# Performance work log

Hardware: AMD Instinct MI355X
Metric: run time of the kernel (lower is better)

Reference implementation:

```python
import jax, jax.numpy as jnp
import numpy as np

N = 50000      # nodes
E = 800000     # edges (before self-loops)
IN = 128       # in_channels
HID = 16       # hidden_channels
HEADS = 8
OUT = 16       # out_channels
NEG_SLOPE = 0.2
BN_EPS = 1e-5
LN_EPS = 1e-5


def setup_inputs() -> dict:
    key = jax.random.key(0)
    ks = jax.random.split(key, 16)
    s = 0.05
    inp = {
        "x": jax.random.normal(ks[0], (N, IN), jnp.float32),
        "edge_index": jax.random.randint(ks[1], (2, E), 0, N, jnp.int64),
        # conv1 (in=IN, out=HID, heads=HEADS, concat=True)
        "Wl1": jax.random.normal(ks[2], (HEADS * HID, IN), jnp.float32) * s,
        "bl1": jnp.zeros((HEADS * HID,), jnp.float32),
        "Wr1": jax.random.normal(ks[3], (HEADS * HID, IN), jnp.float32) * s,
        "br1": jnp.zeros((HEADS * HID,), jnp.float32),
        "att1": jax.random.normal(ks[4], (HEADS, HID), jnp.float32) * s,
        "bias1": jnp.zeros((HEADS * HID,), jnp.float32),
        # batchnorm (eval mode, running stats)
        "bn_w": jnp.ones((HEADS * HID,), jnp.float32),
        "bn_b": jnp.zeros((HEADS * HID,), jnp.float32),
        "bn_rm": jnp.zeros((HEADS * HID,), jnp.float32),
        "bn_rv": jnp.ones((HEADS * HID,), jnp.float32),
        # conv2 (in=HEADS*HID, out=OUT, heads=HEADS, concat=False)
        "Wl2": jax.random.normal(ks[5], (HEADS * OUT, HEADS * HID), jnp.float32) * s,
        "bl2": jnp.zeros((HEADS * OUT,), jnp.float32),
        "Wr2": jax.random.normal(ks[6], (HEADS * OUT, HEADS * HID), jnp.float32) * s,
        "br2": jnp.zeros((HEADS * OUT,), jnp.float32),
        "att2": jax.random.normal(ks[7], (HEADS, OUT), jnp.float32) * s,
        "bias2": jnp.zeros((OUT,), jnp.float32),
        # skip + layernorm
        "Wskip": jax.random.normal(ks[8], (OUT, IN), jnp.float32) * s,
        "ln_w": jnp.ones((OUT,), jnp.float32),
        "ln_b": jnp.zeros((OUT,), jnp.float32),
    }
    return inp


def _gatv2(x, src, dst, Wl, bl, Wr, br, att, bias, heads, ch, concat):
    """PyG GATv2Conv (share_weights=False), eval mode (no dropout)."""
    n = x.shape[0]
    xl = (x @ Wl.T + bl).reshape(n, heads, ch)   # source transform
    xr = (x @ Wr.T + br).reshape(n, heads, ch)   # target transform
    # edge-wise attention score
    e = jax.nn.leaky_relu(xl[src] + xr[dst], NEG_SLOPE)          # [E',H,C]
    score = jnp.einsum('ehc,hc->eh', e, att)                      # [E',H]
    # segment softmax over incoming edges per destination node
    smax = jax.ops.segment_max(score, dst, num_segments=n)
    ex = jnp.exp(score - smax[dst])
    denom = jax.ops.segment_sum(ex, dst, num_segments=n)
    alpha = ex / denom[dst]                                       # [E',H]
    out = jax.ops.segment_sum(alpha[:, :, None] * xl[src], dst, num_segments=n)
    if concat:
        out = out.reshape(n, heads * ch)
    else:
        out = out.mean(axis=1)
    return out + bias


def reference(x, edge_index, Wl1, bl1, Wr1, br1, att1, bias1,
              bn_w, bn_b, bn_rm, bn_rv,
              Wl2, bl2, Wr2, br2, att2, bias2,
              Wskip, ln_w, ln_b):
    n = x.shape[0]
    loops = jnp.arange(n, dtype=edge_index.dtype)
    src = jnp.concatenate([edge_index[0], loops])
    dst = jnp.concatenate([edge_index[1], loops])

    x_res = x @ Wskip.T                                            # [N,OUT]

    h = _gatv2(x, src, dst, Wl1, bl1, Wr1, br1, att1, bias1, HEADS, HID, True)
    # BatchNorm1d in eval mode
    h = (h - bn_rm) * jax.lax.rsqrt(bn_rv + BN_EPS) * bn_w + bn_b
    h = jax.nn.elu(h)

    h = _gatv2(h, src, dst, Wl2, bl2, Wr2, br2, att2, bias2, HEADS, OUT, False)

    y = h + x_res
    mu = y.mean(axis=-1, keepdims=True)
    var = ((y - mu) ** 2).mean(axis=-1, keepdims=True)
    return (y - mu) * jax.lax.rsqrt(var + LN_EPS) * ln_w + ln_b
```

## Files before the change

kernel.cpp:

```cpp
#include <hip/hip_runtime.h>

#define NEG_SLOPE 0.2f
#define BN_EPS 1e-5f
#define LN_EPS 1e-5f

#if __has_builtin(__builtin_amdgcn_exp2f)
#define EXP2F(x) __builtin_amdgcn_exp2f(x)
#else
#define EXP2F(x) exp2f(x)
#endif

typedef __bf16 bf16_t;
typedef bf16_t bf16x8 __attribute__((ext_vector_type(8)));
typedef float floatx4 __attribute__((ext_vector_type(4)));

__device__ __forceinline__ unsigned short f2bf(float f) {
  unsigned u = __float_as_uint(f);
  u += 0x7FFFu + ((u >> 16) & 1u);
  return (unsigned short)(u >> 16);
}
__device__ __forceinline__ float bf_lo(unsigned u) { return __uint_as_float(u << 16); }
__device__ __forceinline__ float bf_hi(unsigned u) { return __uint_as_float(u & 0xFFFF0000u); }

__global__ void cvt_all(const float* __restrict__ x,
                        const float* __restrict__ wl1, const float* __restrict__ wr1,
                        const float* __restrict__ wl2, const float* __restrict__ wr2,
                        const float* __restrict__ wsk,
                        const float* __restrict__ bias1,
                        const float* __restrict__ bn_w, const float* __restrict__ bn_b,
                        const float* __restrict__ bn_rm, const float* __restrict__ bn_rv,
                        const int* __restrict__ ei, int E,
                        unsigned short* __restrict__ xbf,
                        unsigned short* __restrict__ wcat1,
                        unsigned short* __restrict__ wcat2,
                        int* __restrict__ deg8, unsigned short* __restrict__ rpos,
                        float* __restrict__ bnS, float* __restrict__ bnT,
                        int n4x, int N) {
  const int W4 = 128 * 128 / 4;
  const int S4 = 16 * 128 / 4;
  int i = blockIdx.x * blockDim.x + threadIdx.x;
  const float* src;
  unsigned short* dst;
  int j;
  if (i < n4x) { src = x; dst = xbf; j = i; }
  else {
    j = i - n4x;
    if (j < W4)               { src = wl1; dst = wcat1; }
    else if (j < 2 * W4)      { src = wr1; dst = wcat1 + 128 * 128; j -= W4; }
    else if (j < 3 * W4)      { src = wl2; dst = wcat2; j -= 2 * W4; }
    else if (j < 4 * W4)      { src = wr2; dst = wcat2 + 128 * 128; j -= 3 * W4; }
    else if (j < 4 * W4 + S4) { src = wsk; dst = wcat1 + 256 * 128; j -= 4 * W4; }
    else {
      j -= 4 * W4 + S4;
      if (j < 32) {
        for (int t = j * 4; t < j * 4 + 4; ++t) {
          float S = bn_w[t] * rsqrtf(bn_rv[t] + BN_EPS);
          bnS[t] = S;
          bnT[t] = (bias1[t] - bn_rm[t]) * S + bn_b[t];
        }
      } else {
        int e = j - 32;
        if (e < E) {
          int d = ei[E + e];
          int c = (int)(blockIdx.x & 7);
          rpos[e] = (unsigned short)atomicAdd(&deg8[(size_t)c * N + d], 1);
        }
      }
      return;
    }
  }
  float4 v = ((const float4*)src)[j];
  ushort4 o;
  o.x = f2bf(v.x); o.y = f2bf(v.y); o.z = f2bf(v.z); o.w = f2bf(v.w);
  ((ushort4*)dst)[j] = o;
}

__global__ __launch_bounds__(1024)
void csr_scan(const int* __restrict__ deg8, int* __restrict__ meta,
              int* __restrict__ cbase8, int* bsum, int N) {
  __shared__ int wsum[16];
  __shared__ int sh_base;
  int b = blockIdx.x;
  int tid = threadIdx.x;
  int lane = tid & 63, wid = tid >> 6;
  int i0 = b * 4096 + tid * 4;

  int4 v[8];
#pragma unroll
  for (int c = 0; c < 8; ++c) {
    const int* p = deg8 + (size_t)c * N;
    v[c] = make_int4(0, 0, 0, 0);
    if (i0 + 3 < N) v[c] = *(const int4*)(p + i0);
    else if (i0 < N) {
      v[c].x = p[i0];
      if (i0 + 1 < N) v[c].y = p[i0 + 1];
      if (i0 + 2 < N) v[c].z = p[i0 + 2];
    }
  }
  int4 run = make_int4(0, 0, 0, 0);
#pragma unroll
  for (int c = 0; c < 8; ++c) {
    int4 t = v[c];
    v[c] = run;
    run.x += t.x; run.y += t.y; run.z += t.z; run.w += t.w;
  }
  int g1 = (run.x + 1) & ~1, g2 = (run.y + 1) & ~1, g3 = (run.z + 1) & ~1, g4 = (run.w + 1) & ~1;
  int s1 = g1, s2 = s1 + g2, s3 = s2 + g3, s4 = s3 + g4;
  int s = s4;
#pragma unroll
  for (int d = 1; d < 64; d <<= 1) { int t = __shfl_up(s, d, 64); if (lane >= d) s += t; }
  if (lane == 63) wsum[wid] = s;
  __syncthreads();
  if (tid < 16) {
    int ws = wsum[tid];
#pragma unroll
    for (int d = 1; d < 16; d <<= 1) { int t = __shfl_up(ws, d, 16); if (tid >= d) ws += t; }
    wsum[tid] = ws;
  }
  __syncthreads();
  if (tid == 0) {
    __hip_atomic_store(&bsum[b], wsum[15], __ATOMIC_RELEASE, __HIP_MEMORY_SCOPE_AGENT);
    int base = 0;
    for (int j = 0; j < b; ++j) {
      int x;
      do { x = __hip_atomic_load(&bsum[j], __ATOMIC_ACQUIRE, __HIP_MEMORY_SCOPE_AGENT); } while (x < 0);
      base += x;
    }
    sh_base = base;
  }
  __syncthreads();
  int off = sh_base + (wid ? wsum[wid - 1] : 0) + (s - s4);
  int st[4] = {off, off + s1, off + s2, off + s3};
  int tv[4] = {run.x, run.y, run.z, run.w};
#pragma unroll
  for (int k = 0; k < 4; ++k)
    if (i0 + k < N) ((int2*)meta)[i0 + k] = make_int2(st[k], tv[k]);
#pragma unroll
  for (int c = 0; c < 8; ++c) {
    int* p = cbase8 + (size_t)c * N;
    if (i0 + 3 < N) {
      *(int4*)(p + i0) = make_int4(st[0] + v[c].x, st[1] + v[c].y, st[2] + v[c].z, st[3] + v[c].w);
    } else if (i0 < N) {
      p[i0] = st[0] + v[c].x;
      if (i0 + 1 < N) p[i0 + 1] = st[1] + v[c].y;
      if (i0 + 2 < N) p[i0 + 2] = st[2] + v[c].z;
    }
  }
}

__global__ void scatter_edges(const int* __restrict__ ei, int E, int ebase,
                              const int* __restrict__ cbase8,
                              const unsigned short* __restrict__ rpos,
                              unsigned short* __restrict__ csr, int N) {
  int e = blockIdx.x * blockDim.x + threadIdx.x;
  if (e < E) {
    int d = ei[E + e];
    int c = ((ebase + e) >> 8) & 7;
    csr[cbase8[(size_t)c * N + d] + (int)rpos[e]] = (unsigned short)ei[e];
  }
}

template <bool MIXED>
__global__ __launch_bounds__(256)
void gemm_bf16_mfma(const unsigned short* __restrict__ A, const unsigned short* __restrict__ B,
                    const float* __restrict__ bias0, const float* __restrict__ bias1,
                    unsigned short* __restrict__ Cbf, float* __restrict__ Cf,
                    int M, int pstrips) {
  int wave = (int)((blockIdx.x * blockDim.x + threadIdx.x) >> 6);
  int lane = threadIdx.x & 63;
  int mtiles = (M + 31) >> 5;
  if (wave >= mtiles * pstrips) return;
  int mt = wave % mtiles, ps = wave / mtiles;
  int r = lane & 15, quad = lane >> 4;

  const unsigned short* Abase = A + (size_t)(mt * 32 + r) * 128 + quad * 8;
  bf16x8 a0[4], a1[4];
#pragma unroll
  for (int k = 0; k < 4; ++k) {
    a0[k] = *(const bf16x8*)(Abase + 32 * k);
    a1[k] = *(const bf16x8*)(Abase + 16 * 128 + 32 * k);
  }

  int row0 = mt * 32 + quad * 4;
  const int Ptot = MIXED ? 272 : 256;
#pragma unroll
  for (int pp = 0; pp < 4; ++pp) {
    int p0 = ps * 64 + pp * 16;
    if (p0 >= Ptot) break;
    const unsigned short* Bbase = B + (size_t)(p0 + r) * 128 + quad * 8;
    bf16x8 b[4];
#pragma unroll
    for (int k = 0; k < 4; ++k) b[k] = *(const bf16x8*)(Bbase + 32 * k);
    floatx4 acc0 = {0.f, 0.f, 0.f, 0.f};
    floatx4 acc1 = {0.f, 0.f, 0.f, 0.f};
#pragma unroll
    for (int k = 0; k < 4; ++k) {
      acc0 = __builtin_amdgcn_mfma_f32_16x16x32_bf16(a0[k], b[k], acc0, 0, 0, 0);
      acc1 = __builtin_amdgcn_mfma_f32_16x16x32_bf16(a1[k], b[k], acc1, 0, 0, 0);
    }
    int col = p0 + r;
    if (MIXED && col >= 256) {
#pragma unroll
      for (int i = 0; i < 4; ++i) {
        if (row0 + i < M)      Cf[(size_t)(row0 + i) * 16 + (col - 256)] = acc0[i];
        if (row0 + 16 + i < M) Cf[(size_t)(row0 + 16 + i) * 16 + (col - 256)] = acc1[i];
      }
    } else {
      float bs = (col < 128) ? bias0[col] : bias1[col - 128];
#pragma unroll
      for (int i = 0; i < 4; ++i) {
        if (row0 + i < M)      Cbf[(size_t)(row0 + i) * 256 + col] = f2bf(acc0[i] + bs);
        if (row0 + 16 + i < M) Cbf[(size_t)(row0 + 16 + i) * 256 + col] = f2bf(acc1[i] + bs);
      }
    }
  }
}

template <int LAYER>
__global__ __launch_bounds__(256)
void gat_agg(const unsigned int* __restrict__ xlr,
             const int* __restrict__ meta,
             const unsigned short* __restrict__ csr,
             const float* __restrict__ att,
             const float* __restrict__ p0, const float* __restrict__ p1,
             const float* __restrict__ p2, const float* __restrict__ p3,
             void* __restrict__ outp, int n, int nwaves) {
  int lane = threadIdx.x & 63;
  int gw = (int)((blockIdx.x * blockDim.x + threadIdx.x) >> 6);
  int half = lane >> 5, sl = lane & 31;
  float4 at = ((const float4*)att)[sl];
  const float SC = 0.6f * 1.44269504f;
  float a0 = SC * at.x, a1 = SC * at.y, a2 = SC * at.z, a3 = SC * at.w;

  for (int dst = gw; dst < n; dst += nwaves) {
    int dsts = __builtin_amdgcn_readfirstlane(dst);
    int2 m = *(const int2*)(meta + 2 * (size_t)dsts);
    int beg = __builtin_amdgcn_readfirstlane(m.x);
    int dg  = __builtin_amdgcn_readfirstlane(m.y);
    const unsigned* cp = (const unsigned*)csr + (beg >> 1);

    uint2 ur = *(const uint2*)(xlr + (size_t)dsts * 128 + 64 + sl * 2);
    float xr0 = bf_lo(ur.x), xr1 = bf_hi(ur.x), xr2 = bf_lo(ur.y), xr3 = bf_hi(ur.y);
    float lA = 0.f, lB = 0.f;
    float cA0 = 0.f, cA1 = 0.f, cA2 = 0.f, cA3 = 0.f;
    float cB0 = 0.f, cB1 = 0.f, cB2 = 0.f, cB3 = 0.f;

    auto body = [&](uint2 u, float vm, bool useB, bool masked) {
      float x0 = bf_lo(u.x), x1 = bf_hi(u.x), x2 = bf_lo(u.y), x3 = bf_hi(u.y);
      float e0 = x0 + xr0, e1 = x1 + xr1, e2 = x2 + xr2, e3 = x3 + xr3;
      float sc = fmaf(fmaf(fabsf(e0), 0.66666667f, e0), a0,
                 fmaf(fmaf(fabsf(e1), 0.66666667f, e1), a1,
                 fmaf(fmaf(fabsf(e2), 0.66666667f, e2), a2,
                      fmaf(fabsf(e3), 0.66666667f, e3) * a3)));
      sc += __shfl_xor(sc, 1);
      sc += __shfl_xor(sc, 2);
      float pw = EXP2F(sc);
      if (masked) pw *= vm;
      if (useB) {
        lB += pw;
        cB0 = fmaf(pw, x0, cB0); cB1 = fmaf(pw, x1, cB1);
        cB2 = fmaf(pw, x2, cB2); cB3 = fmaf(pw, x3, cB3);
      } else {
        lA += pw;
        cA0 = fmaf(pw, x0, cA0); cA1 = fmaf(pw, x1, cA1);
        cA2 = fmaf(pw, x2, cA2); cA3 = fmaf(pw, x3, cA3);
      }
    };

    int npm = dg >> 1;
    int npm4 = npm & ~3;
    int p = 0;
    for (; p < npm4; p += 4) {
      uint2 u[4];
#pragma unroll
      for (int k = 0; k < 4; ++k) {
        unsigned pr = cp[p + k];
        int s = half ? (int)(pr >> 16) : (int)(pr & 0xFFFFu);
        u[k] = *(const uint2*)(xlr + ((size_t)s << 7) + sl * 2);
      }
#pragma unroll
      for (int k = 0; k < 4; ++k) body(u[k], 1.f, k & 1, false);
    }
    {
      int tot = dg + 1;
      uint2 u[4];
      float vm[4];
#pragma unroll
      for (int k = 0; k < 4; ++k) {
        unsigned pr = cp[p + k];
        int e0 = 2 * (p + k), e1 = e0 + 1;
        int sA = (e0 < dg) ? (int)(pr & 0xFFFFu) : dsts;
        int sB = (e1 < dg) ? (int)(pr >> 16) : dsts;
        float mA = (e0 < tot) ? 1.f : 0.f;
        float mB = (e1 < tot) ? 1.f : 0.f;
        int s = half ? sB : sA;
        vm[k] = half ? mB : mA;
        u[k] = *(const uint2*)(xlr + ((size_t)s << 7) + sl * 2);
      }
#pragma unroll
      for (int k = 0; k < 4; ++k) body(u[k], vm[k], k & 1, true);
    }

    float l = lA + lB;
    float c0 = cA0 + cB0, c1 = cA1 + cB1, c2 = cA2 + cB2, c3 = cA3 + cB3;
    l  += __shfl_xor(l, 32);
    c0 += __shfl_xor(c0, 32); c1 += __shfl_xor(c1, 32);
    c2 += __shfl_xor(c2, 32); c3 += __shfl_xor(c3, 32);
    float inv = 1.f / l;

    if (LAYER == 1) {
      float4 S = ((const float4*)p0)[sl];
      float4 T = ((const float4*)p1)[sl];
      float o0 = fmaf(c0 * inv, S.x, T.x);
      float o1 = fmaf(c1 * inv, S.y, T.y);
      float o2 = fmaf(c2 * inv, S.z, T.z);
      float o3 = fmaf(c3 * inv, S.w, T.w);
      o0 = (o0 > 0.f) ? o0 : (__expf(o0) - 1.f);
      o1 = (o1 > 0.f) ? o1 : (__expf(o1) - 1.f);
      o2 = (o2 > 0.f) ? o2 : (__expf(o2) - 1.f);
      o3 = (o3 > 0.f) ? o3 : (__expf(o3) - 1.f);
      if (half == 0) {
        uint2 o;
        o.x = ((unsigned)f2bf(o1) << 16) | f2bf(o0);
        o.y = ((unsigned)f2bf(o3) << 16) | f2bf(o2);
        ((uint2*)outp)[(size_t)dst * 32 + sl] = o;
      }
    } else {
      float y0 = c0 * inv, y1 = c1 * inv, y2 = c2 * inv, y3 = c3 * inv;
#pragma unroll
      for (int d = 4; d <= 16; d <<= 1) {
        y0 += __shfl_xor(y0, d); y1 += __shfl_xor(y1, d);
        y2 += __shfl_xor(y2, d); y3 += __shfl_xor(y3, d);
      }
      int chh = (sl & 3) * 4;
      float4 b2 = *(const float4*)(p1 + chh);
      float4 xs = *(const float4*)(p0 + (size_t)dst * 16 + chh);
      y0 = y0 * 0.125f + b2.x + xs.x;
      y1 = y1 * 0.125f + b2.y + xs.y;
      y2 = y2 * 0.125f + b2.z + xs.z;
      y3 = y3 * 0.125f + b2.w + xs.w;
      float t = (y0 + y1) + (y2 + y3);
      t += __shfl_xor(t, 1); t += __shfl_xor(t, 2);
      float mu = t * (1.f / 16.f);
      float d0 = y0 - mu, d1 = y1 - mu, d2 = y2 - mu, d3 = y3 - mu;
      float v = (d0 * d0 + d1 * d1) + (d2 * d2 + d3 * d3);
      v += __shfl_xor(v, 1); v += __shfl_xor(v, 2);
      float istd = rsqrtf(v * (1.f / 16.f) + LN_EPS);
      float4 lw = *(const float4*)(p2 + chh);
      float4 lb = *(const float4*)(p3 + chh);
      if (lane < 4) {
        float4 o;
        o.x = d0 * istd * lw.x + lb.x;
        o.y = d1 * istd * lw.y + lb.y;
        o.z = d2 * istd * lw.z + lb.z;
        o.w = d3 * istd * lw.w + lb.w;
        *(float4*)((float*)outp + (size_t)dst * 16 + chh) = o;
      }
    }
  }
}

extern "C" void kernel_launch(void* const* d_in, const int* in_sizes, int n_in,
                              void* d_out, int out_size, void* d_ws, size_t ws_size,
                              hipStream_t stream) {
  const float* x     = (const float*)d_in[0];
  const int*   ei    = (const int*)d_in[1];
  const float* Wl1   = (const float*)d_in[2];
  const float* bl1   = (const float*)d_in[3];
  const float* Wr1   = (const float*)d_in[4];
  const float* br1   = (const float*)d_in[5];
  const float* att1  = (const float*)d_in[6];
  const float* bias1 = (const float*)d_in[7];
  const float* bn_w  = (const float*)d_in[8];
  const float* bn_b  = (const float*)d_in[9];
  const float* bn_rm = (const float*)d_in[10];
  const float* bn_rv = (const float*)d_in[11];
  const float* Wl2   = (const float*)d_in[12];
  const float* bl2   = (const float*)d_in[13];
  const float* Wr2   = (const float*)d_in[14];
  const float* br2   = (const float*)d_in[15];
  const float* att2  = (const float*)d_in[16];
  const float* bias2 = (const float*)d_in[17];
  const float* Wskip = (const float*)d_in[18];
  const float* ln_w  = (const float*)d_in[19];
  const float* ln_b  = (const float*)d_in[20];

  const int N = in_sizes[0] / 128;
  const int E = in_sizes[1] / 2;

  char* w = (char*)d_ws;
  size_t off = 0;
  auto alloc = [&](size_t bytes) -> void* {
    void* p = (void*)(w + off);
    off += (bytes + 255) & ~(size_t)255;
    return p;
  };
  unsigned short* xbf    = (unsigned short*)alloc((size_t)N * 128 * 2);
  unsigned short* wcat1  = (unsigned short*)alloc(272 * 128 * 2);
  unsigned short* wcat2  = (unsigned short*)alloc(256 * 128 * 2);
  unsigned int*   xlr    = (unsigned int*)alloc((size_t)N * 128 * 4);
  float*          xres   = (float*)alloc((size_t)N * 16 * 4);
  unsigned short* hbf    = (unsigned short*)alloc((size_t)N * 128 * 2);
  float*          bnS    = (float*)alloc(128 * 4);
  float*          bnT    = (float*)alloc(128 * 4);
  int*            deg8   = (int*)alloc((size_t)8 * N * 4);
  int*            cbase8 = (int*)alloc((size_t)8 * N * 4);
  int*            meta   = (int*)alloc((size_t)2 * N * 4);
  int*            bsum   = (int*)alloc(64 * 4);
  unsigned short* rpos   = (unsigned short*)alloc((size_t)E * 2);
  unsigned short* csr    = (unsigned short*)alloc((size_t)(E + N) * 2 + 256);

  const int n4x = (N * 128) / 4;
  const int W4 = 128 * 128 / 4, S4 = 16 * 128 / 4;
  const int ebase = n4x + 4 * W4 + S4 + 32;
  const int nb = (N + 4095) / 4096;

  hipMemsetAsync(deg8, 0, (size_t)8 * N * 4, stream);
  hipMemsetAsync(bsum, 0xFF, 64 * 4, stream);
  {
    int tot = ebase + E;
    cvt_all<<<(tot + 255) / 256, 256, 0, stream>>>(
        x, Wl1, Wr1, Wl2, Wr2, Wskip, bias1, bn_w, bn_b, bn_rm, bn_rv, ei, E,
        xbf, wcat1, wcat2, deg8, rpos, bnS, bnT, n4x, N);
  }

  csr_scan<<<nb, 1024, 0, stream>>>(deg8, meta, cbase8, bsum, N);
  scatter_edges<<<(E + 255) / 256, 256, 0, stream>>>(ei, E, ebase, cbase8, rpos, csr, N);

  {
    int mtiles = (N + 31) >> 5;
    int waves = mtiles * 5;
    gemm_bf16_mfma<true><<<(waves + 3) / 4, 256, 0, stream>>>(
        xbf, wcat1, bl1, br1, (unsigned short*)xlr, xres, N, 5);
  }

  {
    int blocks = 2048, nwaves = blocks * 4;
    gat_agg<1><<<blocks, 256, 0, stream>>>(xlr, meta, csr, att1,
                                           bnS, bnT, nullptr, nullptr, (void*)hbf, N, nwaves);
  }

  {
    int mtiles = (N + 31) >> 5;
    int waves = mtiles * 4;
    gemm_bf16_mfma<false><<<(waves + 3) / 4, 256, 0, stream>>>(
        hbf, wcat2, bl2, br2, (unsigned short*)xlr, nullptr, N, 4);
  }

  {
    int blocks = 2048, nwaves = blocks * 4;
    gat_agg<2><<<blocks, 256, 0, stream>>>(xlr, meta, csr, att2,
                                           xres, bias2, ln_w, ln_b, d_out, N, nwaves);
  }
}
```

Baseline: 309.3 us.

## Fuse edge scatter with layer-1 GEMM in one interleaved launch and merge memsets

The CSR edge scatter and the first-layer MFMA GEMM are independent, so they now run in a single kernel whose blocks alternate between scatter work and GEMM tiles. The intent is to overlap the memory-bound scatter with the compute-bound GEMM and drop one kernel launch. The block-sum sentinel changes from -1 to 0 (values stored plus one), and bsum is moved next to deg8 so a single memset clears both. The second GEMM loses its template and the Ptot guard.

```diff
diff --git a/kernel.cpp b/kernel.cpp
--- a/kernel.cpp
+++ b/kernel.cpp
@@ -119,12 +119,12 @@
   }
   __syncthreads();
   if (tid == 0) {
-    __hip_atomic_store(&bsum[b], wsum[15], __ATOMIC_RELEASE, __HIP_MEMORY_SCOPE_AGENT);
+    __hip_atomic_store(&bsum[b], wsum[15] + 1, __ATOMIC_RELEASE, __HIP_MEMORY_SCOPE_AGENT);
     int base = 0;
     for (int j = 0; j < b; ++j) {
       int x;
-      do { x = __hip_atomic_load(&bsum[j], __ATOMIC_ACQUIRE, __HIP_MEMORY_SCOPE_AGENT); } while (x < 0);
-      base += x;
+      do { x = __hip_atomic_load(&bsum[j], __ATOMIC_ACQUIRE, __HIP_MEMORY_SCOPE_AGENT); } while (x == 0);
+      base += x - 1;
     }
     sh_base = base;
   }
@@ -148,24 +148,86 @@
   }
 }
 
-__global__ void scatter_edges(const int* __restrict__ ei, int E, int ebase,
-                              const int* __restrict__ cbase8,
-                              const unsigned short* __restrict__ rpos,
-                              unsigned short* __restrict__ csr, int N) {
-  int e = blockIdx.x * blockDim.x + threadIdx.x;
-  if (e < E) {
-    int d = ei[E + e];
-    int c = ((ebase + e) >> 8) & 7;
-    csr[cbase8[(size_t)c * N + d] + (int)rpos[e]] = (unsigned short)ei[e];
-  }
-}
-
-template <bool MIXED>
+__global__ __launch_bounds__(256)
+void scatter_gemm(const int* __restrict__ ei, int E, int ebase,
+                  const int* __restrict__ cbase8,
+                  const unsigned short* __restrict__ rpos,
+                  unsigned short* __restrict__ csr, int N, int SCB,
+                  const unsigned short* __restrict__ A, const unsigned short* __restrict__ B,
+                  const float* __restrict__ bias0, const float* __restrict__ bias1,
+                  unsigned short* __restrict__ Cbf, float* __restrict__ Cf,
+                  int M, int pstrips, int GMB) {
+  int b = (int)blockIdx.x;
+  int mn2 = 2 * min(SCB, GMB);
+  bool isScatter;
+  int id;
+  if (b < mn2) { isScatter = (b & 1) == 0; id = b >> 1; }
+  else { isScatter = SCB > GMB; id = (b - mn2) + min(SCB, GMB); }
+
+  if (isScatter) {
+    int e = id * 256 + (int)threadIdx.x;
+    if (e < E) {
+      int d = ei[E + e];
+      int c = ((ebase + e) >> 8) & 7;
+      csr[cbase8[(size_t)c * N + d] + (int)rpos[e]] = (unsigned short)ei[e];
+    }
+    return;
+  }
+
+  int wave = id * 4 + (int)(threadIdx.x >> 6);
+  int lane = threadIdx.x & 63;
+  int mtiles = (M + 31) >> 5;
+  if (wave >= mtiles * pstrips) return;
+  int mt = wave % mtiles, ps = wave / mtiles;
+  int r = lane & 15, quad = lane >> 4;
+
+  const unsigned short* Abase = A + (size_t)(mt * 32 + r) * 128 + quad * 8;
+  bf16x8 a0[4], a1[4];
+#pragma unroll
+  for (int k = 0; k < 4; ++k) {
+    a0[k] = *(const bf16x8*)(Abase + 32 * k);
+    a1[k] = *(const bf16x8*)(Abase + 16 * 128 + 32 * k);
+  }
+
+  int row0 = mt * 32 + quad * 4;
+  const int Ptot = 272;
+#pragma unroll
+  for (int pp = 0; pp < 4; ++pp) {
+    int p0 = ps * 64 + pp * 16;
+    if (p0 >= Ptot) break;
+    const unsigned short* Bbase = B + (size_t)(p0 + r) * 128 + quad * 8;
+    bf16x8 bfr[4];
+#pragma unroll
+    for (int k = 0; k < 4; ++k) bfr[k] = *(const bf16x8*)(Bbase + 32 * k);
+    floatx4 acc0 = {0.f, 0.f, 0.f, 0.f};
+    floatx4 acc1 = {0.f, 0.f, 0.f, 0.f};
+#pragma unroll
+    for (int k = 0; k < 4; ++k) {
+      acc0 = __builtin_amdgcn_mfma_f32_16x16x32_bf16(a0[k], bfr[k], acc0, 0, 0, 0);
+      acc1 = __builtin_amdgcn_mfma_f32_16x16x32_bf16(a1[k], bfr[k], acc1, 0, 0, 0);
+    }
+    int col = p0 + r;
+    if (col >= 256) {
+#pragma unroll
+      for (int i = 0; i < 4; ++i) {
+        if (row0 + i < M)      Cf[(size_t)(row0 + i) * 16 + (col - 256)] = acc0[i];
+        if (row0 + 16 + i < M) Cf[(size_t)(row0 + 16 + i) * 16 + (col - 256)] = acc1[i];
+      }
+    } else {
+      float bs = (col < 128) ? bias0[col] : bias1[col - 128];
+#pragma unroll
+      for (int i = 0; i < 4; ++i) {
+        if (row0 + i < M)      Cbf[(size_t)(row0 + i) * 256 + col] = f2bf(acc0[i] + bs);
+        if (row0 + 16 + i < M) Cbf[(size_t)(row0 + 16 + i) * 256 + col] = f2bf(acc1[i] + bs);
+      }
+    }
+  }
+}
+
 __global__ __launch_bounds__(256)
 void gemm_bf16_mfma(const unsigned short* __restrict__ A, const unsigned short* __restrict__ B,
                     const float* __restrict__ bias0, const float* __restrict__ bias1,
-                    unsigned short* __restrict__ Cbf, float* __restrict__ Cf,
-                    int M, int pstrips) {
+                    unsigned short* __restrict__ Cbf, int M, int pstrips) {
   int wave = (int)((blockIdx.x * blockDim.x + threadIdx.x) >> 6);
   int lane = threadIdx.x & 63;
   int mtiles = (M + 31) >> 5;
@@ -182,11 +244,9 @@
   }
 
   int row0 = mt * 32 + quad * 4;
-  const int Ptot = MIXED ? 272 : 256;
 #pragma unroll
   for (int pp = 0; pp < 4; ++pp) {
     int p0 = ps * 64 + pp * 16;
-    if (p0 >= Ptot) break;
     const unsigned short* Bbase = B + (size_t)(p0 + r) * 128 + quad * 8;
     bf16x8 b[4];
 #pragma unroll
@@ -199,19 +259,11 @@
       acc1 = __builtin_amdgcn_mfma_f32_16x16x32_bf16(a1[k], b[k], acc1, 0, 0, 0);
     }
     int col = p0 + r;
-    if (MIXED && col >= 256) {
-#pragma unroll
-      for (int i = 0; i < 4; ++i) {
-        if (row0 + i < M)      Cf[(size_t)(row0 + i) * 16 + (col - 256)] = acc0[i];
-        if (row0 + 16 + i < M) Cf[(size_t)(row0 + 16 + i) * 16 + (col - 256)] = acc1[i];
-      }
-    } else {
-      float bs = (col < 128) ? bias0[col] : bias1[col - 128];
-#pragma unroll
-      for (int i = 0; i < 4; ++i) {
-        if (row0 + i < M)      Cbf[(size_t)(row0 + i) * 256 + col] = f2bf(acc0[i] + bs);
-        if (row0 + 16 + i < M) Cbf[(size_t)(row0 + 16 + i) * 256 + col] = f2bf(acc1[i] + bs);
-      }
+    float bs = (col < 128) ? bias0[col] : bias1[col - 128];
+#pragma unroll
+    for (int i = 0; i < 4; ++i) {
+      if (row0 + i < M)      Cbf[(size_t)(row0 + i) * 256 + col] = f2bf(acc0[i] + bs);
+      if (row0 + 16 + i < M) Cbf[(size_t)(row0 + 16 + i) * 256 + col] = f2bf(acc1[i] + bs);
     }
   }
 }
@@ -404,9 +456,9 @@
   float*          bnS    = (float*)alloc(128 * 4);
   float*          bnT    = (float*)alloc(128 * 4);
   int*            deg8   = (int*)alloc((size_t)8 * N * 4);
+  int*            bsum   = (int*)alloc(64 * 4);
   int*            cbase8 = (int*)alloc((size_t)8 * N * 4);
   int*            meta   = (int*)alloc((size_t)2 * N * 4);
-  int*            bsum   = (int*)alloc(64 * 4);
   unsigned short* rpos   = (unsigned short*)alloc((size_t)E * 2);
   unsigned short* csr    = (unsigned short*)alloc((size_t)(E + N) * 2 + 256);
 
@@ -415,8 +467,7 @@
   const int ebase = n4x + 4 * W4 + S4 + 32;
   const int nb = (N + 4095) / 4096;
 
-  hipMemsetAsync(deg8, 0, (size_t)8 * N * 4, stream);
-  hipMemsetAsync(bsum, 0xFF, 64 * 4, stream);
+  hipMemsetAsync(deg8, 0, (size_t)8 * N * 4 + 256 + 64 * 4, stream);
   {
     int tot = ebase + E;
     cvt_all<<<(tot + 255) / 256, 256, 0, stream>>>(
@@ -425,13 +476,14 @@
   }
 
   csr_scan<<<nb, 1024, 0, stream>>>(deg8, meta, cbase8, bsum, N);
-  scatter_edges<<<(E + 255) / 256, 256, 0, stream>>>(ei, E, ebase, cbase8, rpos, csr, N);
 
   {
+    int SCB = (E + 255) / 256;
     int mtiles = (N + 31) >> 5;
-    int waves = mtiles * 5;
-    gemm_bf16_mfma<true><<<(waves + 3) / 4, 256, 0, stream>>>(
-        xbf, wcat1, bl1, br1, (unsigned short*)xlr, xres, N, 5);
+    int GMB = (mtiles * 5 + 3) / 4;
+    scatter_gemm<<<SCB + GMB, 256, 0, stream>>>(
+        ei, E, ebase, cbase8, rpos, csr, N, SCB,
+        xbf, wcat1, bl1, br1, (unsigned short*)xlr, xres, N, 5, GMB);
   }
 
   {
@@ -443,8 +495,8 @@
   {
     int mtiles = (N + 31) >> 5;
     int waves = mtiles * 4;
-    gemm_bf16_mfma<false><<<(waves + 3) / 4, 256, 0, stream>>>(
-        hbf, wcat2, bl2, br2, (unsigned short*)xlr, nullptr, N, 4);
+    gemm_bf16_mfma<<<(waves + 3) / 4, 256, 0, stream>>>(
+        hbf, wcat2, bl2, br2, (unsigned short*)xlr, N, 4);
   }
 
   {
```

Measured after the change: 313.7 us. No clear change (+1.4%).
